# Kernel optimization log

Hardware: AMD Instinct MI355X
Metric: run time of the kernel (lower is better)

Reference implementation:

```python
import jax, jax.numpy as jnp
import numpy as np

B, T, C, H = 2, 2048, 1024, 16
D = C // H  # head dim 64


def setup_inputs() -> dict:
    key = jax.random.key(0)
    k1, k2, k3, k4, k5 = jax.random.split(key, 5)
    s = 0.02
    return {
        "x": jax.random.normal(k1, (B, T, C), jnp.float32),
        "w_attn": jax.random.normal(k2, (C, 3 * C), jnp.float32) * s,
        "b_attn": jnp.zeros((3 * C,), jnp.float32),
        "w_proj": jax.random.normal(k3, (C, C), jnp.float32) * s,
        "b_proj": jnp.zeros((C,), jnp.float32),
    }


def reference(x, w_attn, b_attn, w_proj, b_proj):
    b, t, c = x.shape
    qkv = x @ w_attn + b_attn  # [B,T,3C]
    q, k, v = jnp.split(qkv, 3, axis=-1)
    # [B,T,C] -> [B,H,T,D]
    q = q.reshape(b, t, H, D).transpose(0, 2, 1, 3)
    k = k.reshape(b, t, H, D).transpose(0, 2, 1, 3)
    v = v.reshape(b, t, H, D).transpose(0, 2, 1, 3)
    scores = jnp.einsum("bhqd,bhkd->bhqk", q, k) * (1.0 / jnp.sqrt(jnp.float32(D)))
    causal = jnp.tril(jnp.ones((t, t), bool))
    scores = jnp.where(causal[None, None], scores, jnp.float32(-jnp.inf))
    attn = jax.nn.softmax(scores, axis=-1)
    out = jnp.einsum("bhqk,bhkd->bhqd", attn, v)  # [B,H,T,D]
    out = out.transpose(0, 2, 1, 3).reshape(b, t, c)
    return out @ w_proj + b_proj
```

## Files before the change

kernel.cpp:

```cpp
#include <hip/hip_runtime.h>
#include <hip/hip_bf16.h>

#define B_ 2
#define T_ 2048
#define C_ 1024
#define H_ 16
#define D_ 64
#define M1 4096
#define N1 3072
#define K_ 1024

typedef __attribute__((ext_vector_type(8))) __bf16 bf16x8;
typedef __attribute__((ext_vector_type(4))) float f32x4;
typedef __attribute__((ext_vector_type(8))) unsigned short ushort8_t;
typedef __attribute__((ext_vector_type(4))) unsigned short ushort4_t;
typedef __attribute__((ext_vector_type(2))) unsigned int uint2_t;

static __device__ __forceinline__ unsigned short f2bf(float f) {
    unsigned int u = __builtin_bit_cast(unsigned int, f);
    u += 0x7fffu + ((u >> 16) & 1u);
    return (unsigned short)(u >> 16);
}
static __device__ __forceinline__ unsigned short f2bf_hw(float f) {
    return __builtin_bit_cast(unsigned short, (__bf16)f);
}
static __device__ __forceinline__ unsigned int packbf(float lo, float hi) {
    return (unsigned int)f2bf_hw(lo) | ((unsigned int)f2bf_hw(hi) << 16);
}
static __device__ __forceinline__ bf16x8 bload(const unsigned short* p) {
    return __builtin_bit_cast(bf16x8, *(const ushort8_t*)p);
}

#if defined(__has_builtin)
#if __has_builtin(__builtin_amdgcn_exp2f)
#define HAVE_EXP2_BUILTIN 1
#endif
#endif
static __device__ __forceinline__ float fexp2(float x) {
#ifdef HAVE_EXP2_BUILTIN
    return __builtin_amdgcn_exp2f(x);
#else
    float r; asm("v_exp_f32 %0, %1" : "=v"(r) : "v"(x)); return r;
#endif
}

typedef __attribute__((address_space(1))) const unsigned int gu32;
typedef __attribute__((address_space(3))) unsigned int lu32;
static __device__ __forceinline__ void gld16(const void* g, void* l) {
    __builtin_amdgcn_global_load_lds((gu32*)g, (lu32*)l, 16, 0, 0);
}

#define VMCNT(n) asm volatile("s_waitcnt vmcnt(" #n ")" ::: "memory")
#define LGKM0    asm volatile("s_waitcnt lgkmcnt(0)" ::: "memory")

__global__ __launch_bounds__(256)
void prologue_kernel(const float* __restrict__ x,
                     const float* __restrict__ w_attn,
                     const float* __restrict__ w_proj,
                     unsigned short* __restrict__ Xb,
                     unsigned short* __restrict__ Wt1,
                     unsigned short* __restrict__ Wt2)
{
    __shared__ float tile[32][33];
    const int blk = blockIdx.x;
    if (blk < 1024) {
        int idx = blk * 256 + threadIdx.x;
        const int n4 = (M1 * K_) / 4;
        for (int i = idx; i < n4; i += 1024 * 256) {
            float4 v = ((const float4*)x)[i];
            ushort4_t o;
            o.x = f2bf(v.x); o.y = f2bf(v.y); o.z = f2bf(v.z); o.w = f2bf(v.w);
            ((ushort4_t*)Xb)[i] = o;
        }
        return;
    }
    const float* in;
    unsigned short* out;
    int N, bx, by;
    if (blk < 4096) {
        in = w_attn; out = Wt1; N = N1;
        int t = blk - 1024;
        bx = t % 96; by = t / 96;
    } else {
        in = w_proj; out = Wt2; N = C_;
        int t = blk - 4096;
        bx = t % 32; by = t / 32;
    }
    int tx = threadIdx.x & 31;
    int ty = threadIdx.x >> 5;
    int n0 = bx * 32;
    int k0 = by * 32;
#pragma unroll
    for (int rr = 0; rr < 32; rr += 8)
        tile[ty + rr][tx] = in[(size_t)(k0 + ty + rr) * N + n0 + tx];
    __syncthreads();
#pragma unroll
    for (int rr = 0; rr < 32; rr += 8)
        out[(size_t)(n0 + ty + rr) * K_ + k0 + tx] = f2bf(tile[tx][ty + rr]);
}

template <bool SWAP>
static __device__ __forceinline__ void gemm_loop8(
    const unsigned short* __restrict__ A, const unsigned short* __restrict__ Bt,
    unsigned short (*As)[128 * 32], unsigned short (*Bs)[128 * 32],
    int row0, int col0, int tid, f32x4 (&acc)[2][4])
{
    const int lane = tid & 63;
    const int wave = tid >> 6;
    const int g = lane >> 4, cl = lane & 15;
    const int wr = (wave & 3) * 32, wc = (wave >> 2) * 64;
    const int srow = tid >> 2;
    const int sgran = tid & 3;
#pragma unroll
    for (int m = 0; m < 2; ++m)
#pragma unroll
        for (int n = 0; n < 4; ++n)
            acc[m][n] = (f32x4){0.f, 0.f, 0.f, 0.f};
    const int lg = sgran ^ ((srow >> 1) & 3);
    auto stage = [&](int buf, int k0) {
        gld16(A + (size_t)(row0 + srow) * K_ + k0 + lg * 8,
              (char*)&As[buf][0] + wave * 1024);
        gld16(Bt + (size_t)(col0 + srow) * K_ + k0 + lg * 8,
              (char*)&Bs[buf][0] + wave * 1024);
    };
    stage(0, 0);
    stage(1, 32);
    for (int t = 0; t < K_ / 32; ++t) {
        const int k0 = t * 32;
        if (k0 + 32 < K_) { VMCNT(2); }
        else              { VMCNT(0); }
        __builtin_amdgcn_s_barrier();
        __builtin_amdgcn_sched_barrier(0);
        if (t + 2 < K_ / 32) stage((t + 2) % 3, k0 + 64);
        const int buf = t % 3;
        bf16x8 af[2], bfv[4];
#pragma unroll
        for (int m = 0; m < 2; ++m) {
            int ra = wr + m * 16 + cl;
            af[m] = bload(&As[buf][ra * 32 + (g ^ ((ra >> 1) & 3)) * 8]);
        }
#pragma unroll
        for (int n = 0; n < 4; ++n) {
            int rb = wc + n * 16 + cl;
            bfv[n] = bload(&Bs[buf][rb * 32 + (g ^ ((rb >> 1) & 3)) * 8]);
        }
#pragma unroll
        for (int m = 0; m < 2; ++m)
#pragma unroll
            for (int n = 0; n < 4; ++n)
                acc[m][n] = SWAP
                    ? __builtin_amdgcn_mfma_f32_16x16x32_bf16(bfv[n], af[m], acc[m][n], 0, 0, 0)
                    : __builtin_amdgcn_mfma_f32_16x16x32_bf16(af[m], bfv[n], acc[m][n], 0, 0, 0);
    }
}

__global__ __launch_bounds__(512, 6)
void gemm_qkv_kernel(const unsigned short* __restrict__ A,
                     const unsigned short* __restrict__ Bt,
                     const float* __restrict__ bias,
                     unsigned short* __restrict__ Qo,
                     unsigned short* __restrict__ Ko,
                     unsigned short* __restrict__ Vt)
{
    __shared__ unsigned short As[3][128 * 32];
    __shared__ unsigned short Bs[3][128 * 32];
    const int lin = blockIdx.x + gridDim.x * blockIdx.y;
    const int xcd = lin & 7;
    const int idx = lin >> 3;
    const int bx = (xcd >> 1) * 8 + (idx & 7);
    const int by = (xcd & 1) * 12 + (idx >> 3);
    const int row0 = bx * 128, col0 = by * 128;

    const int tid = threadIdx.x;
    const int lane = tid & 63;
    const int wave = tid >> 6;
    const int g = lane >> 4, cl = lane & 15;
    const int wr = (wave & 3) * 32, wc = (wave >> 2) * 64;

    f32x4 acc[2][4];
    gemm_loop8<false>(A, Bt, As, Bs, row0, col0, tid, acc);

    const float QSCALE = 0.125f * 1.44269504088896340736f;
#pragma unroll
    for (int m = 0; m < 2; ++m) {
        int i0 = row0 + wr + m * 16 + g * 4;
        int b = i0 >> 11, t0 = i0 & 2047;
#pragma unroll
        for (int n = 0; n < 4; ++n) {
            int j = col0 + wc + n * 16 + cl;
            int which = j >> 10;
            int c = j & 1023;
            int h = c >> 6, d = c & 63;
            float bv = bias[j];
            size_t bh = (size_t)(b * H_ + h);
            float v0 = acc[m][n][0] + bv;
            float v1 = acc[m][n][1] + bv;
            float v2 = acc[m][n][2] + bv;
            float v3 = acc[m][n][3] + bv;
            if (which == 2) {
                uint2_t w;
                w.x = packbf(v0, v1);
                w.y = packbf(v2, v3);
                *(uint2_t*)&Vt[(bh * D_ + d) * T_ + t0] = w;
            } else if (which == 0) {
                Qo[(bh * T_ + t0 + 0) * D_ + d] = f2bf_hw(v0 * QSCALE);
                Qo[(bh * T_ + t0 + 1) * D_ + d] = f2bf_hw(v1 * QSCALE);
                Qo[(bh * T_ + t0 + 2) * D_ + d] = f2bf_hw(v2 * QSCALE);
                Qo[(bh * T_ + t0 + 3) * D_ + d] = f2bf_hw(v3 * QSCALE);
            } else {
                Ko[(bh * T_ + t0 + 0) * D_ + d] = f2bf_hw(v0);
                Ko[(bh * T_ + t0 + 1) * D_ + d] = f2bf_hw(v1);
                Ko[(bh * T_ + t0 + 2) * D_ + d] = f2bf_hw(v2);
                Ko[(bh * T_ + t0 + 3) * D_ + d] = f2bf_hw(v3);
            }
        }
    }
}

__global__ __launch_bounds__(512, 4)
void gemm_proj_kernel(const unsigned short* __restrict__ A,
                      const unsigned short* __restrict__ Bt,
                      const float* __restrict__ bias,
                      float* __restrict__ out)
{
    __shared__ unsigned short As[3][128 * 32];
    __shared__ unsigned short Bs[3][128 * 32];
    const int row0 = blockIdx.x * 128, col0 = blockIdx.y * 128;
    const int tid = threadIdx.x;
    const int lane = tid & 63;
    const int wave = tid >> 6;
    const int g = lane >> 4, cl = lane & 15;
    const int wr = (wave & 3) * 32, wc = (wave >> 2) * 64;

    f32x4 acc[2][4];
    gemm_loop8<true>(A, Bt, As, Bs, row0, col0, tid, acc);

#pragma unroll
    for (int m = 0; m < 2; ++m) {
        int i = row0 + wr + m * 16 + cl;
#pragma unroll
        for (int n = 0; n < 4; ++n) {
            int j0 = col0 + wc + n * 16 + g * 4;
            float4 bv = *(const float4*)&bias[j0];
            f32x4 o = acc[m][n];
            o[0] += bv.x; o[1] += bv.y; o[2] += bv.z; o[3] += bv.w;
            *(f32x4*)&out[(size_t)i * C_ + j0] = o;
        }
    }
}

__global__ __launch_bounds__(256)
void attn_kernel(const unsigned short* __restrict__ Q,
                 const unsigned short* __restrict__ Kb,
                 const unsigned short* __restrict__ Vh_,
                 unsigned short* __restrict__ AO)
{
    __shared__ unsigned short Klds[2][64 * 64];
    __shared__ unsigned short Vlds[2][64 * 64];
    __shared__ unsigned short Plds[4][16 * 64];
    const int lin = blockIdx.x;
    const int idx = lin >> 3;
    const int bh  = (lin & 7) + 8 * (idx & 3);
    const int qt  = 31 - (idx >> 2);
    const int b = bh >> 4, h = bh & 15;
    const int tid = threadIdx.x;
    const int lane = tid & 63;
    const int wave = tid >> 6;
    const int g = lane >> 4, cl = lane & 15;

    const unsigned short* Qh = Q + (size_t)bh * T_ * D_;
    const unsigned short* Kh = Kb + (size_t)bh * T_ * D_;
    const unsigned short* Vh = Vh_ + (size_t)bh * D_ * T_;

    const int srow = tid >> 3;
    const int sg   = tid & 7;
    const int pswz = (cl & 7) << 4;

    auto stage = [&](int bufi, int kb) {
#pragma unroll
        for (int c = 0; c < 2; ++c) {
            int r = srow + c * 32;
            int lg = sg ^ (r & 7);
            gld16(Kh + (size_t)(kb + r) * D_ + lg * 8,
                  (char*)&Klds[bufi][0] + c * 4096 + wave * 1024);
            gld16(Vh + (size_t)r * T_ + kb + lg * 8,
                  (char*)&Vlds[bufi][0] + c * 4096 + wave * 1024);
        }
    };

    const int q0 = qt * 64 + wave * 16;
    const int tq = q0 + cl;

    bf16x8 qf[2];
#pragma unroll
    for (int c2 = 0; c2 < 2; ++c2)
        qf[c2] = bload(Qh + (size_t)(q0 + cl) * D_ + c2 * 32 + g * 8);

    f32x4 oacc[4];
#pragma unroll
    for (int n = 0; n < 4; ++n) oacc[n] = (f32x4){0.f, 0.f, 0.f, 0.f};
    float m_run = -INFINITY;
    float l_part = 0.f;

    auto attn_step = [&](int kb, int buf, bool diag) {
        f32x4 sc[4];
        __builtin_amdgcn_s_setprio(1);
#pragma unroll
        for (int n = 0; n < 4; ++n) {
            sc[n] = (f32x4){0.f, 0.f, 0.f, 0.f};
#pragma unroll
            for (int c2 = 0; c2 < 2; ++c2) {
                int pg = (c2 * 4 + g) ^ (cl & 7);
                bf16x8 kf = bload(&Klds[buf][(n * 16 + cl) * 64 + pg * 8]);
                sc[n] = __builtin_amdgcn_mfma_f32_16x16x32_bf16(kf, qf[c2], sc[n], 0, 0, 0);
            }
        }
        __builtin_amdgcn_s_setprio(0);
        if (diag) {
#pragma unroll
            for (int n = 0; n < 4; ++n) {
                int k4 = kb + n * 16 + g * 4;
#pragma unroll
                for (int r = 0; r < 4; ++r)
                    if (k4 + r > tq) sc[n][r] = -INFINITY;
            }
        }
        float t0 = fmaxf(fmaxf(sc[0][0], sc[0][1]), sc[0][2]);
        float t1 = fmaxf(fmaxf(sc[0][3], sc[1][0]), sc[1][1]);
        float t2 = fmaxf(fmaxf(sc[1][2], sc[1][3]), sc[2][0]);
        float t3 = fmaxf(fmaxf(sc[2][1], sc[2][2]), sc[2][3]);
        float t4 = fmaxf(fmaxf(sc[3][0], sc[3][1]), sc[3][2]);
        float u0 = fmaxf(fmaxf(t0, t1), t2);
        float u1 = fmaxf(fmaxf(t3, t4), sc[3][3]);
        float lm = fmaxf(u0, u1);
        if (!__all(lm <= m_run + 8.f)) {
            float vmax = lm;
            vmax = fmaxf(vmax, __shfl_xor(vmax, 16, 64));
            vmax = fmaxf(vmax, __shfl_xor(vmax, 32, 64));
            float mn = fmaxf(m_run, vmax);
            float alpha = fexp2(m_run - mn);
            l_part *= alpha;
#pragma unroll
            for (int n = 0; n < 4; ++n)
#pragma unroll
                for (int r = 0; r < 4; ++r) oacc[n][r] *= alpha;
            m_run = mn;
        }
        float p[4][4], psub[4];
#pragma unroll
        for (int n = 0; n < 4; ++n) {
#pragma unroll
            for (int r = 0; r < 4; ++r) p[n][r] = fexp2(sc[n][r] - m_run);
            psub[n] = (p[n][0] + p[n][1]) + (p[n][2] + p[n][3]);
        }
        l_part += (psub[0] + psub[1]) + (psub[2] + psub[3]);
#pragma unroll
        for (int n = 0; n < 4; ++n) {
            uint2_t w;
            w.x = packbf(p[n][0], p[n][1]);
            w.y = packbf(p[n][2], p[n][3]);
            *(uint2_t*)((char*)&Plds[wave][0] + ((cl * 128 + n * 32 + g * 8) ^ pswz)) = w;
        }
        bf16x8 pf[2];
#pragma unroll
        for (int kk = 0; kk < 2; ++kk)
            pf[kk] = bload((const unsigned short*)
                ((char*)&Plds[wave][0] + ((cl * 128 + kk * 64 + g * 16) ^ pswz)));
        __builtin_amdgcn_s_setprio(1);
#pragma unroll
        for (int n = 0; n < 4; ++n) {
#pragma unroll
            for (int kk = 0; kk < 2; ++kk) {
                int pg = (kk * 4 + g) ^ (cl & 7);
                bf16x8 vfr = bload(&Vlds[buf][(n * 16 + cl) * 64 + pg * 8]);
                oacc[n] = __builtin_amdgcn_mfma_f32_16x16x32_bf16(vfr, pf[kk], oacc[n], 0, 0, 0);
            }
        }
        __builtin_amdgcn_s_setprio(0);
    };

    stage(0, 0);
    int buf = 0;
    for (int kt = 0; kt < qt; ++kt) {
        VMCNT(0);
        __builtin_amdgcn_s_barrier();
        __builtin_amdgcn_sched_barrier(0);
        stage(buf ^ 1, (kt + 1) * 64);
        attn_step(kt * 64, buf, false);
        buf ^= 1;
    }
    VMCNT(0);
    __builtin_amdgcn_s_barrier();
    __builtin_amdgcn_sched_barrier(0);
    attn_step(qt * 64, buf, true);

    float lt = l_part;
    lt += __shfl_xor(lt, 16, 64);
    lt += __shfl_xor(lt, 32, 64);
    float inv = 1.f / lt;
#pragma unroll
    for (int n = 0; n < 4; ++n) {
        uint2_t w;
        w.x = packbf(oacc[n][0] * inv, oacc[n][1] * inv);
        w.y = packbf(oacc[n][2] * inv, oacc[n][3] * inv);
        *(uint2_t*)&AO[((size_t)b * T_ + tq) * C_ + h * D_ + n * 16 + g * 4] = w;
    }
}

extern "C" void kernel_launch(void* const* d_in, const int* in_sizes, int n_in,
                              void* d_out, int out_size, void* d_ws, size_t ws_size,
                              hipStream_t stream) {
    (void)in_sizes; (void)n_in; (void)out_size; (void)ws_size;
    const float* x      = (const float*)d_in[0];
    const float* w_attn = (const float*)d_in[1];
    const float* b_attn = (const float*)d_in[2];
    const float* w_proj = (const float*)d_in[3];
    const float* b_proj = (const float*)d_in[4];
    float* out = (float*)d_out;

    char* ws = (char*)d_ws;
    unsigned short* Xb  = (unsigned short*)(ws);
    unsigned short* Wt1 = (unsigned short*)(ws + ((size_t)8  << 20));
    unsigned short* Wt2 = (unsigned short*)(ws + ((size_t)14 << 20));
    unsigned short* Qb  = (unsigned short*)(ws + ((size_t)16 << 20));
    unsigned short* Kb  = (unsigned short*)(ws + ((size_t)24 << 20));
    unsigned short* Vt  = (unsigned short*)(ws + ((size_t)32 << 20));
    unsigned short* AO  = Xb;

    prologue_kernel<<<5120, 256, 0, stream>>>(x, w_attn, w_proj, Xb, Wt1, Wt2);
    gemm_qkv_kernel<<<dim3(M1 / 128, N1 / 128), 512, 0, stream>>>(Xb, Wt1, b_attn, Qb, Kb, Vt);
    attn_kernel<<<1024, 256, 0, stream>>>(Qb, Kb, Vt, AO);
    gemm_proj_kernel<<<dim3(M1 / 128, C_ / 128), 512, 0, stream>>>(AO, Wt2, b_proj, out);
}
```

Before: 104.5 us.

## Keep softmax probabilities in registers and permute V loads to match

Removes the per-wave LDS round trip used to transpose the P tile into the MFMA B-operand layout. The probabilities are packed straight from the score accumulator registers, and the V fragment loads are reordered, as two 8-byte LDS reads per MFMA, so the reduction index matches that register layout. This saves LDS writes and reads plus shared memory per step, but doubles the number of V LDS read instructions and relies on the index permutation being consistent.

```diff
diff --git a/kernel.cpp b/kernel.cpp
--- a/kernel.cpp
+++ b/kernel.cpp
@@ -15,6 +15,7 @@
 typedef __attribute__((ext_vector_type(8))) unsigned short ushort8_t;
 typedef __attribute__((ext_vector_type(4))) unsigned short ushort4_t;
 typedef __attribute__((ext_vector_type(2))) unsigned int uint2_t;
+typedef __attribute__((ext_vector_type(4))) unsigned int uint4_t;
 
 static __device__ __forceinline__ unsigned short f2bf(float f) {
     unsigned int u = __builtin_bit_cast(unsigned int, f);
@@ -257,7 +258,6 @@
 {
     __shared__ unsigned short Klds[2][64 * 64];
     __shared__ unsigned short Vlds[2][64 * 64];
-    __shared__ unsigned short Plds[4][16 * 64];
     const int lin = blockIdx.x;
     const int idx = lin >> 3;
     const int bh  = (lin & 7) + 8 * (idx & 3);
@@ -274,7 +274,6 @@
 
     const int srow = tid >> 3;
     const int sg   = tid & 7;
-    const int pswz = (cl & 7) << 4;
 
     auto stage = [&](int bufi, int kb) {
 #pragma unroll
@@ -347,33 +346,42 @@
             m_run = mn;
         }
         float p[4][4], psub[4];
+        unsigned int pw[4][2];
 #pragma unroll
         for (int n = 0; n < 4; ++n) {
 #pragma unroll
             for (int r = 0; r < 4; ++r) p[n][r] = fexp2(sc[n][r] - m_run);
             psub[n] = (p[n][0] + p[n][1]) + (p[n][2] + p[n][3]);
+            pw[n][0] = packbf(p[n][0], p[n][1]);
+            pw[n][1] = packbf(p[n][2], p[n][3]);
         }
         l_part += (psub[0] + psub[1]) + (psub[2] + psub[3]);
-#pragma unroll
-        for (int n = 0; n < 4; ++n) {
-            uint2_t w;
-            w.x = packbf(p[n][0], p[n][1]);
-            w.y = packbf(p[n][2], p[n][3]);
-            *(uint2_t*)((char*)&Plds[wave][0] + ((cl * 128 + n * 32 + g * 8) ^ pswz)) = w;
-        }
         bf16x8 pf[2];
 #pragma unroll
-        for (int kk = 0; kk < 2; ++kk)
-            pf[kk] = bload((const unsigned short*)
-                ((char*)&Plds[wave][0] + ((cl * 128 + kk * 64 + g * 16) ^ pswz)));
+        for (int kk = 0; kk < 2; ++kk) {
+            uint4_t w;
+            w.x = pw[2 * kk][0];
+            w.y = pw[2 * kk][1];
+            w.z = pw[2 * kk + 1][0];
+            w.w = pw[2 * kk + 1][1];
+            pf[kk] = __builtin_bit_cast(bf16x8, w);
+        }
         __builtin_amdgcn_s_setprio(1);
 #pragma unroll
         for (int n = 0; n < 4; ++n) {
+            const char* vbase = (const char*)&Vlds[buf][0]
+                              + (n * 16 + cl) * 128 + (g & 1) * 8;
 #pragma unroll
             for (int kk = 0; kk < 2; ++kk) {
-                int pg = (kk * 4 + g) ^ (cl & 7);
-                bf16x8 vfr = bload(&Vlds[buf][(n * 16 + cl) * 64 + pg * 8]);
-                oacc[n] = __builtin_amdgcn_mfma_f32_16x16x32_bf16(vfr, pf[kk], oacc[n], 0, 0, 0);
+                ushort4_t lo = *(const ushort4_t*)(vbase +
+                    (((4 * kk + (g >> 1)) ^ (cl & 7)) * 16));
+                ushort4_t hi = *(const ushort4_t*)(vbase +
+                    (((4 * kk + 2 + (g >> 1)) ^ (cl & 7)) * 16));
+                ushort8_t v8;
+                v8[0] = lo[0]; v8[1] = lo[1]; v8[2] = lo[2]; v8[3] = lo[3];
+                v8[4] = hi[0]; v8[5] = hi[1]; v8[6] = hi[2]; v8[7] = hi[3];
+                oacc[n] = __builtin_amdgcn_mfma_f32_16x16x32_bf16(
+                    __builtin_bit_cast(bf16x8, v8), pf[kk], oacc[n], 0, 0, 0);
             }
         }
         __builtin_amdgcn_s_setprio(0);
```

Result: no change. 106.5 us (+2.0%).
